# Kernel optimization log

Hardware: AMD Instinct MI355X
Metric: run time of the kernel (lower is better)

## Reference

```python
import jax, jax.numpy as jnp
import numpy as np

TOP_K = 2  # config.num_experts_per_tok


def setup_inputs() -> dict:
    key = jax.random.key(0)
    ks = jax.random.split(key, 5)
    B, S, H, F, E = 1, 2048, 2048, 1408, 8
    sc_h = 1.0 / np.sqrt(H)
    sc_f = 1.0 / np.sqrt(F)
    return {
        "hidden_states": jax.random.normal(ks[0], (B, S, H), jnp.float32),
        "gate_w": jax.random.normal(ks[1], (E, H), jnp.float32) * sc_h,
        "w1": jax.random.normal(ks[2], (E, F, H), jnp.float32) * sc_h,
        "w3": jax.random.normal(ks[3], (E, F, H), jnp.float32) * sc_h,
        "w2": jax.random.normal(ks[4], (E, H, F), jnp.float32) * sc_f,
    }


def reference(hidden_states, gate_w, w1, w3, w2):
    B, S, H = hidden_states.shape
    x = hidden_states.reshape(-1, H)            # [T, H]
    T = x.shape[0]
    E = gate_w.shape[0]

    # Router: logits -> fp32 softmax -> top-k -> renormalize
    router_logits = x @ gate_w.T                # [T, E]
    probs = jax.nn.softmax(router_logits.astype(jnp.float32), axis=-1)
    topk_w, topk_idx = jax.lax.top_k(probs, TOP_K)          # [T, K]
    topk_w = topk_w / topk_w.sum(axis=-1, keepdims=True)
    topk_w = topk_w.astype(x.dtype)

    # Scatter top-k weights into a dense [T, E] combine matrix (zero elsewhere)
    w_full = jnp.zeros((T, E), x.dtype).at[jnp.arange(T)[:, None], topk_idx].add(topk_w)

    # Per-expert SwiGLU MLP applied to all tokens; masked combine honors routing.
    g = jnp.einsum('th,efh->etf', x, w1)        # [E, T, F]
    u = jnp.einsum('th,efh->etf', x, w3)        # [E, T, F]
    h = jax.nn.silu(g) * u                      # [E, T, F]
    y = jnp.einsum('etf,ehf->eth', h, w2)       # [E, T, H]
    out = jnp.einsum('eth,te->th', y, w_full)   # [T, H]

    final_hidden_states = out.reshape(B, S, H)
    return final_hidden_states, router_logits
```

## Files before the change

### kernel.cpp

```cpp
#include <hip/hip_runtime.h>
#include <hip/hip_bf16.h>

#define T_TOK 2048
#define H_DIM 2048
#define F_DIM 1408
#define N_EXP 8
#define BM 128
#define BN 64
#define BK 64

#define NITEM 40
#define G1_NY (F_DIM / BN)
#define G2_NY (H_DIM / BN)
#define G1_CHUNK ((NITEM * G1_NY) / 8)
#define G2_CHUNK ((NITEM * G2_NY) / 8)

typedef float f32x4 __attribute__((ext_vector_type(4)));
typedef short s16x8 __attribute__((ext_vector_type(8)));
typedef unsigned int u32;

#define LOFF(row, kbyte) (((row) << 7) + ((kbyte) ^ (((row) & 7) << 4)))

__device__ __forceinline__ int bf2i(__hip_bfloat162 h) {
  int r; __builtin_memcpy(&r, &h, 4); return r;
}

__device__ __forceinline__ int4 pack8(float4 a, float4 b) {
  int4 r;
  r.x = bf2i(__float22bfloat162_rn(float2{a.x, a.y}));
  r.y = bf2i(__float22bfloat162_rn(float2{a.z, a.w}));
  r.z = bf2i(__float22bfloat162_rn(float2{b.x, b.y}));
  r.w = bf2i(__float22bfloat162_rn(float2{b.z, b.w}));
  return r;
}

__device__ __forceinline__ unsigned short f2bf(float f) {
  __hip_bfloat16 h = __float2bfloat16(f);
  unsigned short r; __builtin_memcpy(&r, &h, 2); return r;
}

__device__ __forceinline__ f32x4 mfma16(s16x8 a, s16x8 b, f32x4 c) {
  return __builtin_amdgcn_mfma_f32_16x16x32_bf16(a, b, c, 0, 0, 0);
}

__device__ __forceinline__ void dma16(const unsigned short* g, unsigned short* l) {
  __builtin_amdgcn_global_load_lds((const __attribute__((address_space(1))) u32*)g,
                                   (__attribute__((address_space(3))) u32*)l, 16, 0, 0);
}

__global__ void router_kernel(const float* __restrict__ x, const float* __restrict__ gw,
                              float* __restrict__ logits, int* __restrict__ tk_idx,
                              float* __restrict__ tk_w, unsigned short* __restrict__ xb) {
  __shared__ float xs[H_DIM];
  __shared__ float lg[N_EXP];
  const int t = blockIdx.x;
  const int tid = threadIdx.x;
  const float4 xv = ((const float4*)(x + (size_t)t * H_DIM))[tid];
  ((float4*)xs)[tid] = xv;
  int2 cw;
  cw.x = bf2i(__float22bfloat162_rn(float2{xv.x, xv.y}));
  cw.y = bf2i(__float22bfloat162_rn(float2{xv.z, xv.w}));
  ((int2*)(xb + (size_t)t * H_DIM))[tid] = cw;
  __syncthreads();
  const int w = tid >> 6, l = tid & 63;
  const float* g = gw + w * H_DIM;
  float s = 0.f;
  for (int j = l; j < H_DIM; j += 64) s += xs[j] * g[j];
#pragma unroll
  for (int o = 32; o; o >>= 1) s += __shfl_down(s, o);
  if (l == 0) lg[w] = s;
  __syncthreads();
  if (tid == 0) {
    float mx = lg[0];
#pragma unroll
    for (int i = 1; i < N_EXP; i++) mx = fmaxf(mx, lg[i]);
    float p[N_EXP];
#pragma unroll
    for (int i = 0; i < N_EXP; i++) p[i] = __expf(lg[i] - mx);
    int i0 = 0;
#pragma unroll
    for (int i = 1; i < N_EXP; i++) if (p[i] > p[i0]) i0 = i;
    int i1 = (i0 == 0) ? 1 : 0;
#pragma unroll
    for (int i = 0; i < N_EXP; i++) if (i != i0 && p[i] > p[i1]) i1 = i;
    const float ww = p[i0] + p[i1];
    tk_idx[t * 2] = i0; tk_idx[t * 2 + 1] = i1;
    tk_w[t * 2] = p[i0] / ww; tk_w[t * 2 + 1] = p[i1] / ww;
#pragma unroll
    for (int i = 0; i < N_EXP; i++) logits[t * N_EXP + i] = lg[i];
  }
}

__global__ void build_lists(const int* __restrict__ tk_idx, const float* __restrict__ tk_w,
                            int* __restrict__ counts, int* __restrict__ entries,
                            float* __restrict__ wlist) {
  const int e = blockIdx.x;
  const int l = threadIdx.x;
  int base = 0;
  for (int t0 = 0; t0 < T_TOK; t0 += 64) {
    const int t = t0 + l;
    int sel = -1; float w = 0.f;
    const int i0 = tk_idx[t * 2], i1 = tk_idx[t * 2 + 1];
    if (i0 == e) { sel = t * 2; w = tk_w[t * 2]; }
    else if (i1 == e) { sel = t * 2 + 1; w = tk_w[t * 2 + 1]; }
    const unsigned long long mask = __ballot(sel >= 0);
    const int pos = base + __popcll(mask & ((1ull << l) - 1ull));
    if (sel >= 0) { entries[e * T_TOK + pos] = sel; wlist[e * T_TOK + pos] = w; }
    base += __popcll(mask);
  }
  if (l == 0) counts[e] = base;
}

__global__ void build_items(const int* __restrict__ counts, int* __restrict__ items) {
  if (threadIdx.x == 0) {
    int n = 0;
#pragma unroll
    for (int e = 0; e < N_EXP; e++) {
      const int c = counts[e];
      for (int m0 = 0; m0 < c; m0 += BM) items[1 + n++] = (e << 16) | (m0 / BM);
    }
    items[0] = n;
  }
}

#define G1_STEP(SARD, SAWR, RB1, RB3, KA1_, KB2_)                             \
  {                                                                           \
    asm volatile("s_waitcnt vmcnt(4) lgkmcnt(0)" ::: "memory");               \
    __builtin_amdgcn_s_barrier();                                             \
    *(int4*)(sB1c + offB) = pack8(RB1[0], RB1[1]);                            \
    *(int4*)(sB3c + offB) = pack8(RB3[0], RB3[1]);                            \
    {                                                                         \
      const int ka = (KA1_);                                                  \
      dma16(ga0 + ka, (SAWR) + aw);                                           \
      dma16(ga1 + ka, (SAWR) + aw + 512);                                     \
    }                                                                         \
    {                                                                         \
      const int kbl = (KB2_);                                                 \
      RB1[0] = *(const float4*)(pb1 + kbl);                                   \
      RB1[1] = *(const float4*)(pb1 + kbl + 4);                               \
      RB3[0] = *(const float4*)(pb3 + kbl);                                   \
      RB3[1] = *(const float4*)(pb3 + kbl + 4);                               \
    }                                                                         \
    asm volatile("s_waitcnt lgkmcnt(0)" ::: "memory");                        \
    __builtin_amdgcn_s_barrier();                                             \
    _Pragma("unroll")                                                         \
    for (int kk = 0; kk < 2; kk++) {                                          \
      const int kbyte = kk * 64 + kb;                                         \
      const s16x8 a0 = *(const s16x8*)((const char*)(SARD) + LOFF(rowA0, kbyte)); \
      const s16x8 a1 = *(const s16x8*)((const char*)(SARD) + LOFF(rowA1, kbyte)); \
      const s16x8 p0 = *(const s16x8*)(sB1c + LOFF(rowB0, kbyte));            \
      const s16x8 p1 = *(const s16x8*)(sB1c + LOFF(rowB1, kbyte));            \
      const s16x8 q0 = *(const s16x8*)(sB3c + LOFF(rowB0, kbyte));            \
      const s16x8 q1 = *(const s16x8*)(sB3c + LOFF(rowB1, kbyte));            \
      aG[0][0] = mfma16(a0, p0, aG[0][0]); aG[0][1] = mfma16(a0, p1, aG[0][1]); \
      aG[1][0] = mfma16(a1, p0, aG[1][0]); aG[1][1] = mfma16(a1, p1, aG[1][1]); \
      aU[0][0] = mfma16(a0, q0, aU[0][0]); aU[0][1] = mfma16(a0, q1, aU[0][1]); \
      aU[1][0] = mfma16(a1, q0, aU[1][0]); aU[1][1] = mfma16(a1, q1, aU[1][1]); \
    }                                                                         \
  }

__global__ __launch_bounds__(512)
void moe_gemm1(const float* __restrict__ w1, const float* __restrict__ w3,
               const unsigned short* __restrict__ xb,
               const int* __restrict__ counts, const int* __restrict__ entries,
               const int* __restrict__ items,
               unsigned short* __restrict__ hb) {
  const int lin = blockIdx.x;
  const int virt = (lin & 7) * G1_CHUNK + (lin >> 3);
  const int ix = virt % NITEM;
  const int iy = virt / NITEM;
  if (ix >= items[0]) return;
  const int it = items[1 + ix];
  const int e = it >> 16;
  const int m0 = (it & 0xffff) * BM;
  const int rem = counts[e] - m0;
  const int n0 = iy * BN;

  __shared__ unsigned short sA[2][BM * BK];
  __shared__ unsigned short sB1[BN * BK];
  __shared__ unsigned short sB3[BN * BK];
  char* sB1c = (char*)sB1; char* sB3c = (char*)sB3;

  const int tid = threadIdx.x;
  const int lane = tid & 63;
  const int wave = tid >> 6;
  const int wm = wave >> 1, wn = wave & 1;

  const int* elist = entries + e * T_TOK + m0;

  const int r0 = tid >> 3;
  const int gc = tid & 7;
  const float* pb1 = w1 + ((size_t)e * F_DIM + n0 + r0) * H_DIM + gc * 8;
  const float* pb3 = w3 + ((size_t)e * F_DIM + n0 + r0) * H_DIM + gc * 8;
  const int offB = LOFF(r0, gc * 16);

  const int arow0 = wave * 16 + (lane >> 3);
  const int arow1 = arow0 + 8;
  const int gcolb = (((lane & 7) << 4) ^ (((lane >> 3) & 7) << 4));
  const int tokA0 = elist[arow0 < rem ? arow0 : 0] >> 1;
  const int tokA1 = elist[arow1 < rem ? arow1 : 0] >> 1;
  const unsigned short* ga0 = xb + (size_t)tokA0 * H_DIM + (gcolb >> 1);
  const unsigned short* ga1 = xb + (size_t)tokA1 * H_DIM + (gcolb >> 1);
  const int aw = wave * 1024;

  const int rowA0 = wm * 32 + (lane & 15);
  const int rowA1 = rowA0 + 16;
  const int rowB0 = wn * 32 + (lane & 15);
  const int rowB1 = rowB0 + 16;
  const int kb = (lane >> 4) * 16;

  const f32x4 zero = {0.f, 0.f, 0.f, 0.f};
  f32x4 aG[2][2], aU[2][2];
#pragma unroll
  for (int i = 0; i < 2; i++)
#pragma unroll
    for (int j = 0; j < 2; j++) { aG[i][j] = zero; aU[i][j] = zero; }

  dma16(ga0, sA[0] + aw);
  dma16(ga1, sA[0] + aw + 512);
  float4 P1[2], P3[2], Q1[2], Q3[2];
  P1[0] = *(const float4*)(pb1);      P1[1] = *(const float4*)(pb1 + 4);
  P3[0] = *(const float4*)(pb3);      P3[1] = *(const float4*)(pb3 + 4);
  Q1[0] = *(const float4*)(pb1 + BK); Q1[1] = *(const float4*)(pb1 + BK + 4);
  Q3[0] = *(const float4*)(pb3 + BK); Q3[1] = *(const float4*)(pb3 + BK + 4);

  const int NT = H_DIM / BK;
  for (int t = 0; t < NT; t += 2) {
    const int ka1 = (t + 1 < NT) ? (t + 1) * BK : 0;
    const int ka2 = (t + 2 < NT) ? (t + 2) * BK : 0;
    const int kb2 = ka2;
    const int kb3 = (t + 3 < NT) ? (t + 3) * BK : 0;
    G1_STEP(sA[0], sA[1], P1, P3, ka1, kb2);
    G1_STEP(sA[1], sA[0], Q1, Q3, ka2, kb3);
  }

#pragma unroll
  for (int i = 0; i < 2; i++) {
#pragma unroll
    for (int r = 0; r < 4; r++) {
      const int m = wm * 32 + i * 16 + ((lane >> 4) << 2) + r;
      if (m < rem) {
        const int entry = elist[m];
        unsigned short* hp = hb + (size_t)entry * F_DIM + n0 + wn * 32 + (lane & 15);
#pragma unroll
        for (int j = 0; j < 2; j++) {
          const float g = aG[i][j][r];
          const float u = aU[i][j][r];
          hp[j * 16] = f2bf(g / (1.f + __expf(-g)) * u);
        }
      }
    }
  }
}

#define G2_STEP(SARD, SAWR, RB, KA1_, KB2_)                                   \
  {                                                                           \
    asm volatile("s_waitcnt vmcnt(2) lgkmcnt(0)" ::: "memory");               \
    __builtin_amdgcn_s_barrier();                                             \
    *(int4*)(sBc + offB) = pack8(RB[0], RB[1]);                               \
    {                                                                         \
      const int ka = (KA1_);                                                  \
      dma16(ga0 + ka, (SAWR) + aw);                                           \
      dma16(ga1 + ka, (SAWR) + aw + 512);                                     \
    }                                                                         \
    {                                                                         \
      const int kbl = (KB2_);                                                 \
      RB[0] = *(const float4*)(pb + kbl);                                     \
      RB[1] = *(const float4*)(pb + kbl + 4);                                 \
    }                                                                         \
    asm volatile("s_waitcnt lgkmcnt(0)" ::: "memory");                        \
    __builtin_amdgcn_s_barrier();                                             \
    _Pragma("unroll")                                                         \
    for (int kk = 0; kk < 2; kk++) {                                          \
      const int kbyte = kk * 64 + kb;                                         \
      const s16x8 a0 = *(const s16x8*)((const char*)(SARD) + LOFF(rowA0, kbyte)); \
      const s16x8 a1 = *(const s16x8*)((const char*)(SARD) + LOFF(rowA1, kbyte)); \
      const s16x8 f0 = *(const s16x8*)(sBc + LOFF(rowB0, kbyte));             \
      const s16x8 f1 = *(const s16x8*)(sBc + LOFF(rowB1, kbyte));             \
      ac[0][0] = mfma16(a0, f0, ac[0][0]); ac[0][1] = mfma16(a0, f1, ac[0][1]); \
      ac[1][0] = mfma16(a1, f0, ac[1][0]); ac[1][1] = mfma16(a1, f1, ac[1][1]); \
    }                                                                         \
  }

__global__ __launch_bounds__(512)
void moe_gemm2(const float* __restrict__ w2,
               const unsigned short* __restrict__ hb,
               const int* __restrict__ counts, const int* __restrict__ entries,
               const float* __restrict__ wlist, const int* __restrict__ items,
               float* __restrict__ out) {
  const int lin = blockIdx.x;
  const int virt = (lin & 7) * G2_CHUNK + (lin >> 3);
  const int ix = virt % NITEM;
  const int iy = virt / NITEM;
  if (ix >= items[0]) return;
  const int it = items[1 + ix];
  const int e = it >> 16;
  const int m0 = (it & 0xffff) * BM;
  const int rem = counts[e] - m0;
  const int n0 = iy * BN;

  __shared__ unsigned short sA[2][BM * BK];
  __shared__ unsigned short sB[BN * BK];
  char* sBc = (char*)sB;

  const int tid = threadIdx.x;
  const int lane = tid & 63;
  const int wave = tid >> 6;
  const int wm = wave >> 1, wn = wave & 1;

  const int* elist = entries + e * T_TOK + m0;
  const float* wl = wlist + e * T_TOK + m0;

  const int r0 = tid >> 3;
  const int gc = tid & 7;
  const float* pb = w2 + ((size_t)e * H_DIM + n0 + r0) * F_DIM + gc * 8;
  const int offB = LOFF(r0, gc * 16);

  const int arow0 = wave * 16 + (lane >> 3);
  const int arow1 = arow0 + 8;
  const int gcolb = (((lane & 7) << 4) ^ (((lane >> 3) & 7) << 4));
  const int enA0 = elist[arow0 < rem ? arow0 : 0];
  const int enA1 = elist[arow1 < rem ? arow1 : 0];
  const unsigned short* ga0 = hb + (size_t)enA0 * F_DIM + (gcolb >> 1);
  const unsigned short* ga1 = hb + (size_t)enA1 * F_DIM + (gcolb >> 1);
  const int aw = wave * 1024;

  const int rowA0 = wm * 32 + (lane & 15);
  const int rowA1 = rowA0 + 16;
  const int rowB0 = wn * 32 + (lane & 15);
  const int rowB1 = rowB0 + 16;
  const int kb = (lane >> 4) * 16;

  const f32x4 zero = {0.f, 0.f, 0.f, 0.f};
  f32x4 ac[2][2];
#pragma unroll
  for (int i = 0; i < 2; i++)
#pragma unroll
    for (int j = 0; j < 2; j++) ac[i][j] = zero;

  dma16(ga0, sA[0] + aw);
  dma16(ga1, sA[0] + aw + 512);
  float4 P[2], Q[2];
  P[0] = *(const float4*)(pb);      P[1] = *(const float4*)(pb + 4);
  Q[0] = *(const float4*)(pb + BK); Q[1] = *(const float4*)(pb + BK + 4);

  const int NT = F_DIM / BK;
  for (int t = 0; t < NT; t += 2) {
    const int ka1 = (t + 1 < NT) ? (t + 1) * BK : 0;
    const int ka2 = (t + 2 < NT) ? (t + 2) * BK : 0;
    const int kb2 = ka2;
    const int kb3 = (t + 3 < NT) ? (t + 3) * BK : 0;
    G2_STEP(sA[0], sA[1], P, ka1, kb2);
    G2_STEP(sA[1], sA[0], Q, ka2, kb3);
  }

#pragma unroll
  for (int i = 0; i < 2; i++) {
#pragma unroll
    for (int r = 0; r < 4; r++) {
      const int m = wm * 32 + i * 16 + ((lane >> 4) << 2) + r;
      if (m < rem) {
        const int entry = elist[m];
        const int tok = entry >> 1;
        const float wgt = wl[m];
        float* op = out + (size_t)tok * H_DIM + n0 + wn * 32 + (lane & 15);
#pragma unroll
        for (int j = 0; j < 2; j++) atomicAdd(op + j * 16, wgt * ac[i][j][r]);
      }
    }
  }
}

extern "C" void kernel_launch(void* const* d_in, const int* in_sizes, int n_in,
                              void* d_out, int out_size, void* d_ws, size_t ws_size,
                              hipStream_t stream) {
  const float* x  = (const float*)d_in[0];
  const float* gw = (const float*)d_in[1];
  const float* w1 = (const float*)d_in[2];
  const float* w3 = (const float*)d_in[3];
  const float* w2 = (const float*)d_in[4];
  float* out = (float*)d_out;
  float* logits = out + (size_t)T_TOK * H_DIM;

  char* ws = (char*)d_ws;
  size_t off = 0;
  unsigned short* xb = (unsigned short*)(ws + off); off += (size_t)T_TOK * H_DIM * 2;
  unsigned short* hb = (unsigned short*)(ws + off); off += (size_t)T_TOK * 2 * F_DIM * 2;
  int*   tk_idx = (int*)(ws + off);   off += (size_t)T_TOK * 2 * 4;
  float* tk_w   = (float*)(ws + off); off += (size_t)T_TOK * 2 * 4;
  int*   counts = (int*)(ws + off);   off += 256;
  int*   entries = (int*)(ws + off);  off += (size_t)N_EXP * T_TOK * 4;
  float* wlist  = (float*)(ws + off); off += (size_t)N_EXP * T_TOK * 4;
  int*   items  = (int*)(ws + off);   off += 256;

  (void)hipMemsetAsync(d_out, 0, (size_t)out_size * sizeof(float), stream);
  router_kernel<<<dim3(T_TOK), 512, 0, stream>>>(x, gw, logits, tk_idx, tk_w, xb);
  build_lists<<<dim3(N_EXP), 64, 0, stream>>>(tk_idx, tk_w, counts, entries, wlist);
  build_items<<<dim3(1), 64, 0, stream>>>(counts, items);
  moe_gemm1<<<dim3(NITEM * G1_NY), 512, 0, stream>>>(w1, w3, xb, counts, entries, items, hb);
  moe_gemm2<<<dim3(NITEM * G2_NY), 512, 0, stream>>>(w2, hb, counts, entries, wlist, items, out);
}
```

Measured before the change: 233.6 us.

## Double-buffer B tiles in LDS to drop one barrier per k-step

Both MoE GEMM kernels now keep two LDS buffers for the weight (B) tile, so the next tile is written into the alternate buffer while MFMAs read the current one. This removes the second lgkmcnt wait and barrier in each k-step, and cuts register prefetch from two stages to one. In exchange it adds a full vmcnt(0) wait before each LDS store, which exposes global-load latency (the previous code waited on vmcnt(4)/vmcnt(2)). It also raises LDS use per block, which may reduce occupancy.

```diff
diff --git a/kernel.cpp b/kernel.cpp
--- a/kernel.cpp
+++ b/kernel.cpp
@@ -123,35 +123,32 @@
   }
 }
 
-#define G1_STEP(SARD, SAWR, RB1, RB3, KA1_, KB2_)                             \
+#define G1_STEP(SARD, SAWR, SB1RD, SB1WR, SB3RD, SB3WR, KA1_, KB2_)           \
   {                                                                           \
-    asm volatile("s_waitcnt vmcnt(4) lgkmcnt(0)" ::: "memory");               \
+    asm volatile("s_waitcnt lgkmcnt(0)" ::: "memory");                        \
     __builtin_amdgcn_s_barrier();                                             \
-    *(int4*)(sB1c + offB) = pack8(RB1[0], RB1[1]);                            \
-    *(int4*)(sB3c + offB) = pack8(RB3[0], RB3[1]);                            \
+    asm volatile("s_waitcnt vmcnt(0)" ::: "memory");                          \
+    *(int4*)((SB1WR) + offB) = pack8(rb1[0], rb1[1]);                         \
+    *(int4*)((SB3WR) + offB) = pack8(rb3[0], rb3[1]);                         \
     {                                                                         \
       const int ka = (KA1_);                                                  \
       dma16(ga0 + ka, (SAWR) + aw);                                           \
       dma16(ga1 + ka, (SAWR) + aw + 512);                                     \
+      const int kbl = (KB2_);                                                 \
+      rb1[0] = *(const float4*)(pb1 + kbl);                                   \
+      rb1[1] = *(const float4*)(pb1 + kbl + 4);                               \
+      rb3[0] = *(const float4*)(pb3 + kbl);                                   \
+      rb3[1] = *(const float4*)(pb3 + kbl + 4);                               \
     }                                                                         \
-    {                                                                         \
-      const int kbl = (KB2_);                                                 \
-      RB1[0] = *(const float4*)(pb1 + kbl);                                   \
-      RB1[1] = *(const float4*)(pb1 + kbl + 4);                               \
-      RB3[0] = *(const float4*)(pb3 + kbl);                                   \
-      RB3[1] = *(const float4*)(pb3 + kbl + 4);                               \
-    }                                                                         \
-    asm volatile("s_waitcnt lgkmcnt(0)" ::: "memory");                        \
-    __builtin_amdgcn_s_barrier();                                             \
     _Pragma("unroll")                                                         \
     for (int kk = 0; kk < 2; kk++) {                                          \
       const int kbyte = kk * 64 + kb;                                         \
       const s16x8 a0 = *(const s16x8*)((const char*)(SARD) + LOFF(rowA0, kbyte)); \
       const s16x8 a1 = *(const s16x8*)((const char*)(SARD) + LOFF(rowA1, kbyte)); \
-      const s16x8 p0 = *(const s16x8*)(sB1c + LOFF(rowB0, kbyte));            \
-      const s16x8 p1 = *(const s16x8*)(sB1c + LOFF(rowB1, kbyte));            \
-      const s16x8 q0 = *(const s16x8*)(sB3c + LOFF(rowB0, kbyte));            \
-      const s16x8 q1 = *(const s16x8*)(sB3c + LOFF(rowB1, kbyte));            \
+      const s16x8 p0 = *(const s16x8*)((SB1RD) + LOFF(rowB0, kbyte));         \
+      const s16x8 p1 = *(const s16x8*)((SB1RD) + LOFF(rowB1, kbyte));         \
+      const s16x8 q0 = *(const s16x8*)((SB3RD) + LOFF(rowB0, kbyte));         \
+      const s16x8 q1 = *(const s16x8*)((SB3RD) + LOFF(rowB1, kbyte));         \
       aG[0][0] = mfma16(a0, p0, aG[0][0]); aG[0][1] = mfma16(a0, p1, aG[0][1]); \
       aG[1][0] = mfma16(a1, p0, aG[1][0]); aG[1][1] = mfma16(a1, p1, aG[1][1]); \
       aU[0][0] = mfma16(a0, q0, aU[0][0]); aU[0][1] = mfma16(a0, q1, aU[0][1]); \
@@ -177,9 +174,10 @@
   const int n0 = iy * BN;
 
   __shared__ unsigned short sA[2][BM * BK];
-  __shared__ unsigned short sB1[BN * BK];
-  __shared__ unsigned short sB3[BN * BK];
-  char* sB1c = (char*)sB1; char* sB3c = (char*)sB3;
+  __shared__ unsigned short sB1[2][BN * BK];
+  __shared__ unsigned short sB3[2][BN * BK];
+  char* sb10 = (char*)sB1[0]; char* sb11 = (char*)sB1[1];
+  char* sb30 = (char*)sB3[0]; char* sb31 = (char*)sB3[1];
 
   const int tid = threadIdx.x;
   const int lane = tid & 63;
@@ -216,22 +214,24 @@
 #pragma unroll
     for (int j = 0; j < 2; j++) { aG[i][j] = zero; aU[i][j] = zero; }
 
+  float4 rb1[2], rb3[2];
   dma16(ga0, sA[0] + aw);
   dma16(ga1, sA[0] + aw + 512);
-  float4 P1[2], P3[2], Q1[2], Q3[2];
-  P1[0] = *(const float4*)(pb1);      P1[1] = *(const float4*)(pb1 + 4);
-  P3[0] = *(const float4*)(pb3);      P3[1] = *(const float4*)(pb3 + 4);
-  Q1[0] = *(const float4*)(pb1 + BK); Q1[1] = *(const float4*)(pb1 + BK + 4);
-  Q3[0] = *(const float4*)(pb3 + BK); Q3[1] = *(const float4*)(pb3 + BK + 4);
+  rb1[0] = *(const float4*)(pb1);      rb1[1] = *(const float4*)(pb1 + 4);
+  rb3[0] = *(const float4*)(pb3);      rb3[1] = *(const float4*)(pb3 + 4);
+  asm volatile("s_waitcnt vmcnt(0)" ::: "memory");
+  *(int4*)(sb10 + offB) = pack8(rb1[0], rb1[1]);
+  *(int4*)(sb30 + offB) = pack8(rb3[0], rb3[1]);
+  rb1[0] = *(const float4*)(pb1 + BK); rb1[1] = *(const float4*)(pb1 + BK + 4);
+  rb3[0] = *(const float4*)(pb3 + BK); rb3[1] = *(const float4*)(pb3 + BK + 4);
 
   const int NT = H_DIM / BK;
   for (int t = 0; t < NT; t += 2) {
     const int ka1 = (t + 1 < NT) ? (t + 1) * BK : 0;
     const int ka2 = (t + 2 < NT) ? (t + 2) * BK : 0;
-    const int kb2 = ka2;
     const int kb3 = (t + 3 < NT) ? (t + 3) * BK : 0;
-    G1_STEP(sA[0], sA[1], P1, P3, ka1, kb2);
-    G1_STEP(sA[1], sA[0], Q1, Q3, ka2, kb3);
+    G1_STEP(sA[0], sA[1], sb10, sb11, sb30, sb31, ka1, ka2);
+    G1_STEP(sA[1], sA[0], sb11, sb10, sb31, sb30, ka2, kb3);
   }
 
 #pragma unroll
@@ -253,30 +253,27 @@
   }
 }
 
-#define G2_STEP(SARD, SAWR, RB, KA1_, KB2_)                                   \
+#define G2_STEP(SARD, SAWR, SBRD, SBWR, KA1_, KB2_)                           \
   {                                                                           \
-    asm volatile("s_waitcnt vmcnt(2) lgkmcnt(0)" ::: "memory");               \
+    asm volatile("s_waitcnt lgkmcnt(0)" ::: "memory");                        \
     __builtin_amdgcn_s_barrier();                                             \
-    *(int4*)(sBc + offB) = pack8(RB[0], RB[1]);                               \
+    asm volatile("s_waitcnt vmcnt(0)" ::: "memory");                          \
+    *(int4*)((SBWR) + offB) = pack8(rb[0], rb[1]);                            \
     {                                                                         \
       const int ka = (KA1_);                                                  \
       dma16(ga0 + ka, (SAWR) + aw);                                           \
       dma16(ga1 + ka, (SAWR) + aw + 512);                                     \
+      const int kbl = (KB2_);                                                 \
+      rb[0] = *(const float4*)(pb + kbl);                                     \
+      rb[1] = *(const float4*)(pb + kbl + 4);                                 \
     }                                                                         \
-    {                                                                         \
-      const int kbl = (KB2_);                                                 \
-      RB[0] = *(const float4*)(pb + kbl);                                     \
-      RB[1] = *(const float4*)(pb + kbl + 4);                                 \
-    }                                                                         \
-    asm volatile("s_waitcnt lgkmcnt(0)" ::: "memory");                        \
-    __builtin_amdgcn_s_barrier();                                             \
     _Pragma("unroll")                                                         \
     for (int kk = 0; kk < 2; kk++) {                                          \
       const int kbyte = kk * 64 + kb;                                         \
       const s16x8 a0 = *(const s16x8*)((const char*)(SARD) + LOFF(rowA0, kbyte)); \
       const s16x8 a1 = *(const s16x8*)((const char*)(SARD) + LOFF(rowA1, kbyte)); \
-      const s16x8 f0 = *(const s16x8*)(sBc + LOFF(rowB0, kbyte));             \
-      const s16x8 f1 = *(const s16x8*)(sBc + LOFF(rowB1, kbyte));             \
+      const s16x8 f0 = *(const s16x8*)((SBRD) + LOFF(rowB0, kbyte));          \
+      const s16x8 f1 = *(const s16x8*)((SBRD) + LOFF(rowB1, kbyte));          \
       ac[0][0] = mfma16(a0, f0, ac[0][0]); ac[0][1] = mfma16(a0, f1, ac[0][1]); \
       ac[1][0] = mfma16(a1, f0, ac[1][0]); ac[1][1] = mfma16(a1, f1, ac[1][1]); \
     }                                                                         \
@@ -300,8 +297,8 @@
   const int n0 = iy * BN;
 
   __shared__ unsigned short sA[2][BM * BK];
-  __shared__ unsigned short sB[BN * BK];
-  char* sBc = (char*)sB;
+  __shared__ unsigned short sB[2][BN * BK];
+  char* sb0 = (char*)sB[0]; char* sb1 = (char*)sB[1];
 
   const int tid = threadIdx.x;
   const int lane = tid & 63;
@@ -338,20 +335,21 @@
 #pragma unroll
     for (int j = 0; j < 2; j++) ac[i][j] = zero;
 
+  float4 rb[2];
   dma16(ga0, sA[0] + aw);
   dma16(ga1, sA[0] + aw + 512);
-  float4 P[2], Q[2];
-  P[0] = *(const float4*)(pb);      P[1] = *(const float4*)(pb + 4);
-  Q[0] = *(const float4*)(pb + BK); Q[1] = *(const float4*)(pb + BK + 4);
+  rb[0] = *(const float4*)(pb);      rb[1] = *(const float4*)(pb + 4);
+  asm volatile("s_waitcnt vmcnt(0)" ::: "memory");
+  *(int4*)(sb0 + offB) = pack8(rb[0], rb[1]);
+  rb[0] = *(const float4*)(pb + BK); rb[1] = *(const float4*)(pb + BK + 4);
 
   const int NT = F_DIM / BK;
   for (int t = 0; t < NT; t += 2) {
     const int ka1 = (t + 1 < NT) ? (t + 1) * BK : 0;
     const int ka2 = (t + 2 < NT) ? (t + 2) * BK : 0;
-    const int kb2 = ka2;
     const int kb3 = (t + 3 < NT) ? (t + 3) * BK : 0;
-    G2_STEP(sA[0], sA[1], P, ka1, kb2);
-    G2_STEP(sA[1], sA[0], Q, ka2, kb3);
+    G2_STEP(sA[0], sA[1], sb0, sb1, ka1, ka2);
+    G2_STEP(sA[1], sA[0], sb1, sb0, ka2, kb3);
   }
 
 #pragma unroll
```

Measured after the change: 521.9 us. 123% more time.
